# Performance work log

Measured on AMD Instinct MI355X. Metric: run time of the kernel, lower is better.

## Reference

```python
import jax, jax.numpy as jnp
import numpy as np

EXPERT_NUM = 64
EXPERT_USE = 8
AUX_LOSS_LAMBDA = 0.01


def setup_inputs() -> dict:
    key = jax.random.key(0)
    k1, k2 = jax.random.split(key)
    h = jax.random.normal(k1, (4, 4096, 2048), dtype=jnp.float32)
    # nn.Linear(embed_dim, expert_num) weight: [expert_num, embed_dim], ~U(-1/sqrt(d), 1/sqrt(d))
    bound = 1.0 / np.sqrt(2048.0)
    W = jax.random.uniform(k2, (EXPERT_NUM, 2048), dtype=jnp.float32,
                           minval=-bound, maxval=bound)
    return {"h": h, "W": W}


def reference(h, W):
    b, s, d = h.shape
    hf = h.reshape(-1, d)                              # [b*s, d]
    logits = jnp.einsum('nd,ed->ne', hf, W)            # [b*s, E]
    scores = jax.nn.softmax(logits, axis=-1)           # [b*s, E]
    expert_scores, expert_ids = jax.lax.top_k(scores, EXPERT_USE)  # [b*s, k]
    expert_weight = expert_scores / jnp.sum(expert_scores, axis=-1, keepdims=True)
    # L2 load-balance aux loss (training mode, lambda > 0)
    seq_probs = scores.reshape(b, s, EXPERT_NUM).mean(axis=1)      # [b, E]
    aux_loss = jnp.mean(jnp.sum(seq_probs ** 2, axis=-1)) * EXPERT_NUM * AUX_LOSS_LAMBDA
    return expert_ids, expert_weight, aux_loss
```

## Files before the change

kernel.cpp:

```cpp
#include <hip/hip_runtime.h>
#include <math.h>

#define NTOK 16384
#define DIM 2048
#define NEXP 64
#define TOPK 8
#define BT 64
#define KC 64
#define NCHUNK (DIM / KC)
#define PADK 68
#define EPW 4

typedef float f2 __attribute__((ext_vector_type(2)));
typedef float f4 __attribute__((ext_vector_type(4)));

__device__ __forceinline__ f2 pk_mul_sv(f2 bs, f2 av) {
    f2 d; asm("v_pk_mul_f32 %0, %1, %2" : "=v"(d) : "s"(bs), "v"(av)); return d;
}
__device__ __forceinline__ f2 pk_add(f2 a, f2 b) {
    f2 d; asm("v_pk_add_f32 %0, %1, %2" : "=v"(d) : "v"(a), "v"(b)); return d;
}

__global__ __launch_bounds__(512, 4) void moe_gemm(
    const float* __restrict__ h, const float* __restrict__ W,
    float* __restrict__ lgout)
{
#pragma clang fp contract(off)
    __shared__ float sA[2][BT * PADK];

    const int tid  = threadIdx.x;
    const int lane = tid & 63;
    const int wv   = tid >> 6;
    const int tile = blockIdx.x >> 1;
    const int hf   = blockIdx.x & 1;
    const long tok0 = (long)tile * BT;
    const float* hA = h + tok0 * DIM;

    const int e0 = __builtin_amdgcn_readfirstlane(hf * 32 + wv * EPW);
    const float* wb = W + (long)e0 * DIM;

    const int rs0 = tid >> 4;
    const int cs0 = (tid & 15) * 4;

    f4 ra = *(const f4*)(hA + (long)rs0 * DIM + cs0);
    f4 rb = *(const f4*)(hA + (long)(rs0 + 32) * DIM + cs0);
    *(f4*)&sA[0][rs0 * PADK + cs0]        = ra;
    *(f4*)&sA[0][(rs0 + 32) * PADK + cs0] = rb;
    ra = *(const f4*)(hA + (long)rs0 * DIM + KC + cs0);
    rb = *(const f4*)(hA + (long)(rs0 + 32) * DIM + KC + cs0);

    f2 a01[EPW], a23[EPW];
    #pragma unroll
    for (int j = 0; j < EPW; ++j) { a01[j] = (f2)(0.f); a23[j] = (f2)(0.f); }

    for (int kc = 0; kc < NCHUNK; ++kc) {
        __syncthreads();
        const int cur = kc & 1;

        if (kc + 1 < NCHUNK) {
            *(f4*)&sA[cur ^ 1][rs0 * PADK + cs0]        = ra;
            *(f4*)&sA[cur ^ 1][(rs0 + 32) * PADK + cs0] = rb;
        }
        if (kc + 2 < NCHUNK) {
            const long ko = (long)(kc + 2) * KC;
            ra = *(const f4*)(hA + (long)rs0 * DIM + ko + cs0);
            rb = *(const f4*)(hA + (long)(rs0 + 32) * DIM + ko + cs0);
        }

        #pragma unroll
        for (int s = 0; s < 4; ++s) {
            const int kb = kc * KC + s * 16;

            f4 B[EPW][4];
            #pragma unroll
            for (int j = 0; j < EPW; ++j)
                #pragma unroll
                for (int q = 0; q < 4; ++q)
                    B[j][q] = *(const f4*)(wb + (long)j * DIM + kb + 4 * q);

            f4 af[4];
            const float* ab = &sA[cur][lane * PADK + s * 16];
            #pragma unroll
            for (int v = 0; v < 4; ++v) af[v] = *(const f4*)(ab + 4 * v);

            f2 alo[4], ahi[4];
            #pragma unroll
            for (int v = 0; v < 4; ++v) {
                alo[v] = __builtin_shufflevector(af[v], af[v], 0, 1);
                ahi[v] = __builtin_shufflevector(af[v], af[v], 2, 3);
            }

            #pragma unroll
            for (int j = 0; j < EPW; ++j) {
                f2 blo[4], bhi[4];
                #pragma unroll
                for (int v = 0; v < 4; ++v) {
                    blo[v] = __builtin_shufflevector(B[j][v], B[j][v], 0, 1);
                    bhi[v] = __builtin_shufflevector(B[j][v], B[j][v], 2, 3);
                }
                f2 t;
                t = pk_add(pk_mul_sv(blo[3], alo[3]), a01[j]);
                t = pk_add(pk_mul_sv(blo[2], alo[2]), t);
                t = pk_add(pk_mul_sv(blo[1], alo[1]), t);
                a01[j] = pk_add(pk_mul_sv(blo[0], alo[0]), t);
                t = pk_add(pk_mul_sv(bhi[3], ahi[3]), a23[j]);
                t = pk_add(pk_mul_sv(bhi[2], ahi[2]), t);
                t = pk_add(pk_mul_sv(bhi[1], ahi[1]), t);
                a23[j] = pk_add(pk_mul_sv(bhi[0], ahi[0]), t);
            }
        }
    }

    #pragma unroll
    for (int j = 0; j < EPW; ++j) {
        f2 s2 = pk_add(a01[j], a23[j]);
        lgout[(tok0 + lane) * NEXP + e0 + j] = s2.x + s2.y;
    }
}

__global__ __launch_bounds__(512) void softmax_topk(
    const float* __restrict__ lgout, float* __restrict__ out,
    float* __restrict__ wsum)
{
    __shared__ float ls[8][NEXP + 2];
    const int tid  = threadIdx.x;
    const int lane = tid & 63;
    const int wv8  = tid >> 6;
    const int blk  = blockIdx.x;
    const long tok0 = (long)blk * 64;
    float auxacc = 0.f;

    for (int tt = 0; tt < 8; ++tt) {
        const long gt = tok0 + wv8 * 8 + tt;
        const float s = lgout[gt * NEXP + lane];

        float m = s;
        #pragma unroll
        for (int off = 32; off >= 1; off >>= 1)
            m = fmaxf(m, __shfl_xor(m, off));

        const float p = expf(s - m);
        ls[wv8][lane] = p;
        __asm__ volatile("" ::: "memory");

        float r0s = ls[wv8][0], r1s = ls[wv8][1], r2s = ls[wv8][2], r3s = ls[wv8][3];
        float r4s = ls[wv8][4], r5s = ls[wv8][5], r6s = ls[wv8][6], r7s = ls[wv8][7];
        #pragma unroll
        for (int i = 1; i < 8; ++i) {
            r0s += ls[wv8][8 * i + 0]; r1s += ls[wv8][8 * i + 1];
            r2s += ls[wv8][8 * i + 2]; r3s += ls[wv8][8 * i + 3];
            r4s += ls[wv8][8 * i + 4]; r5s += ls[wv8][8 * i + 5];
            r6s += ls[wv8][8 * i + 6]; r7s += ls[wv8][8 * i + 7];
        }
        const float S = ((r0s + r1s) + (r2s + r3s)) + ((r4s + r5s) + (r6s + r7s));

        const float score = p / S;
        auxacc += score;

        float cv = score;
        float myv = 0.f;
        int   myi = 0;
        #pragma unroll
        for (int i = 0; i < TOPK; ++i) {
            float v = cv;
            int idx = lane;
            #pragma unroll
            for (int off = 32; off >= 1; off >>= 1) {
                float v2 = __shfl_xor(v, off);
                int   i2 = __shfl_xor(idx, off);
                if (v2 > v || (v2 == v && i2 < idx)) { v = v2; idx = i2; }
            }
            if (lane == i)   { myv = v; myi = idx; }
            if (lane == idx) cv = -1.f;
        }

        float S8 = 0.f;
        #pragma unroll
        for (int r = 0; r < TOPK; ++r) S8 += __shfl(myv, r);

        if (lane < TOPK) {
            const long o = gt * TOPK + lane;
            out[o]                     = (float)myi;
            out[(long)NTOK * TOPK + o] = myv / S8;
        }
    }

    atomicAdd(&wsum[(blk >> 6) * NEXP + lane], auxacc);
}

__global__ __launch_bounds__(1024, 1) void moe_gate_np(
    const float* __restrict__ h, const float* __restrict__ W,
    float* __restrict__ out, float* __restrict__ wsum)
{
#pragma clang fp contract(off)
    __shared__ float sA[BT * PADK];
    __shared__ float lg[BT][NEXP + 2];

    const int tid  = threadIdx.x;
    const int lane = tid & 63;
    const int wv   = tid >> 6;
    const int blk  = blockIdx.x;
    const long tok0 = (long)blk * BT;
    const float* hA = h + tok0 * DIM;

    const int e0 = __builtin_amdgcn_readfirstlane(wv) * EPW;
    const float* wb = W + (long)e0 * DIM;

    const int rs = tid >> 4;
    const int cs = (tid & 15) * 4;
    f4 pa = *(const f4*)(hA + (long)rs * DIM + cs);

    f2 a01[EPW], a23[EPW];
    #pragma unroll
    for (int j = 0; j < EPW; ++j) { a01[j] = (f2)(0.f); a23[j] = (f2)(0.f); }

    for (int kc = 0; kc < NCHUNK; ++kc) {
        __syncthreads();
        *(f4*)&sA[rs * PADK + cs] = pa;
        __syncthreads();
        if (kc + 1 < NCHUNK)
            pa = *(const f4*)(hA + (long)rs * DIM + (long)(kc + 1) * KC + cs);

        #pragma unroll
        for (int s = 0; s < 4; ++s) {
            const int kb = kc * KC + s * 16;
            f4 B[EPW][4];
            #pragma unroll
            for (int j = 0; j < EPW; ++j)
                #pragma unroll
                for (int q = 0; q < 4; ++q)
                    B[j][q] = *(const f4*)(wb + (long)j * DIM + kb + 4 * q);
            f4 af[4];
            const float* ab = &sA[lane * PADK + s * 16];
            #pragma unroll
            for (int v = 0; v < 4; ++v) af[v] = *(const f4*)(ab + 4 * v);
            f2 alo[4], ahi[4];
            #pragma unroll
            for (int v = 0; v < 4; ++v) {
                alo[v] = __builtin_shufflevector(af[v], af[v], 0, 1);
                ahi[v] = __builtin_shufflevector(af[v], af[v], 2, 3);
            }
            #pragma unroll
            for (int j = 0; j < EPW; ++j) {
                f2 blo[4], bhi[4];
                #pragma unroll
                for (int v = 0; v < 4; ++v) {
                    blo[v] = __builtin_shufflevector(B[j][v], B[j][v], 0, 1);
                    bhi[v] = __builtin_shufflevector(B[j][v], B[j][v], 2, 3);
                }
                f2 t;
                t = pk_add(pk_mul_sv(blo[3], alo[3]), a01[j]);
                t = pk_add(pk_mul_sv(blo[2], alo[2]), t);
                t = pk_add(pk_mul_sv(blo[1], alo[1]), t);
                a01[j] = pk_add(pk_mul_sv(blo[0], alo[0]), t);
                t = pk_add(pk_mul_sv(bhi[3], ahi[3]), a23[j]);
                t = pk_add(pk_mul_sv(bhi[2], ahi[2]), t);
                t = pk_add(pk_mul_sv(bhi[1], ahi[1]), t);
                a23[j] = pk_add(pk_mul_sv(bhi[0], ahi[0]), t);
            }
        }
    }

    #pragma unroll
    for (int j = 0; j < EPW; ++j) {
        f2 s2 = pk_add(a01[j], a23[j]);
        lg[lane][e0 + j] = s2.x + s2.y;
    }
    __syncthreads();

    float auxacc = 0.f;
    for (int tt = 0; tt < 4; ++tt) {
        const int t = wv * 4 + tt;
        const float s = lg[t][lane];
        float m = s;
        #pragma unroll
        for (int off = 32; off >= 1; off >>= 1)
            m = fmaxf(m, __shfl_xor(m, off));
        const float p = expf(s - m);
        lg[t][lane] = p;
        __asm__ volatile("" ::: "memory");
        float r0s = lg[t][0], r1s = lg[t][1], r2s = lg[t][2], r3s = lg[t][3];
        float r4s = lg[t][4], r5s = lg[t][5], r6s = lg[t][6], r7s = lg[t][7];
        #pragma unroll
        for (int i = 1; i < 8; ++i) {
            r0s += lg[t][8 * i + 0]; r1s += lg[t][8 * i + 1];
            r2s += lg[t][8 * i + 2]; r3s += lg[t][8 * i + 3];
            r4s += lg[t][8 * i + 4]; r5s += lg[t][8 * i + 5];
            r6s += lg[t][8 * i + 6]; r7s += lg[t][8 * i + 7];
        }
        const float S = ((r0s + r1s) + (r2s + r3s)) + ((r4s + r5s) + (r6s + r7s));
        const float score = p / S;
        auxacc += score;
        float cv = score;
        float myv = 0.f;
        int   myi = 0;
        #pragma unroll
        for (int i = 0; i < TOPK; ++i) {
            float v = cv;
            int idx = lane;
            #pragma unroll
            for (int off = 32; off >= 1; off >>= 1) {
                float v2 = __shfl_xor(v, off);
                int   i2 = __shfl_xor(idx, off);
                if (v2 > v || (v2 == v && i2 < idx)) { v = v2; idx = i2; }
            }
            if (lane == i)   { myv = v; myi = idx; }
            if (lane == idx) cv = -1.f;
        }
        float S8 = 0.f;
        #pragma unroll
        for (int r = 0; r < TOPK; ++r) S8 += __shfl(myv, r);
        if (lane < TOPK) {
            const long o = (tok0 + t) * TOPK + lane;
            out[o]                     = (float)myi;
            out[(long)NTOK * TOPK + o] = myv / S8;
        }
    }
    atomicAdd(&wsum[(blk >> 6) * NEXP + lane], auxacc);
}

__global__ void aux_finish(const float* __restrict__ wsum, float* __restrict__ out)
{
    const int lane = threadIdx.x;
    float a = 0.f;
    #pragma unroll
    for (int b = 0; b < 4; ++b) {
        const float v = wsum[b * NEXP + lane] * (1.0f / 4096.0f);
        a = fmaf(v, v, a);
    }
    #pragma unroll
    for (int off = 32; off >= 1; off >>= 1)
        a += __shfl_xor(a, off);
    if (lane == 0)
        out[2L * NTOK * TOPK] = a * 0.25f * (float)NEXP * 0.01f;
}

extern "C" void kernel_launch(void* const* d_in, const int* in_sizes, int n_in,
                              void* d_out, int out_size, void* d_ws, size_t ws_size,
                              hipStream_t stream) {
    const float* h = (const float*)d_in[0];
    const float* W = (const float*)d_in[1];
    float* out  = (float*)d_out;
    float* wsum = (float*)d_ws;

    const size_t need = 4096 + (size_t)NTOK * NEXP * sizeof(float);

    hipMemsetAsync(d_ws, 0, 1024, stream);
    if (ws_size >= need) {
        float* lgout = (float*)((char*)d_ws + 4096);
        moe_gemm<<<(NTOK / BT) * 2, 512, 0, stream>>>(h, W, lgout);
        softmax_topk<<<NTOK / 64, 512, 0, stream>>>(lgout, out, wsum);
    } else {
        moe_gate_np<<<NTOK / BT, 1024, 0, stream>>>(h, W, out, wsum);
    }
    aux_finish<<<1, 64, 0, stream>>>(wsum, out);
}
```

Measured before the change: 164.0 us.

## Fuse softmax/top-k and aux-loss finish into GEMM kernel via per-tile completion flags

After: 336.6 us. +105.2%, slower.

```diff
diff --git a/kernel.cpp b/kernel.cpp
--- a/kernel.cpp
+++ b/kernel.cpp
@@ -10,6 +10,7 @@
 #define NCHUNK (DIM / KC)
 #define PADK 68
 #define EPW 4
+#define NTILE (NTOK / BT)
 
 typedef float f2 __attribute__((ext_vector_type(2)));
 typedef float f4 __attribute__((ext_vector_type(4)));
@@ -21,12 +22,15 @@
     f2 d; asm("v_pk_add_f32 %0, %1, %2" : "=v"(d) : "v"(a), "v"(b)); return d;
 }
 
-__global__ __launch_bounds__(512, 4) void moe_gemm(
+__global__ __launch_bounds__(512, 4) void moe_gemm_fused(
     const float* __restrict__ h, const float* __restrict__ W,
-    float* __restrict__ lgout)
+    float* __restrict__ out, float* __restrict__ wsum,
+    int* __restrict__ flags, float* __restrict__ lgout)
 {
 #pragma clang fp contract(off)
     __shared__ float sA[2][BT * PADK];
+    __shared__ float ls[8][NEXP + 2];
+    __shared__ int swin, sdone;
 
     const int tid  = threadIdx.x;
     const int lane = tid & 63;
@@ -116,23 +120,18 @@
         f2 s2 = pk_add(a01[j], a23[j]);
         lgout[(tok0 + lane) * NEXP + e0 + j] = s2.x + s2.y;
     }
-}
-
-__global__ __launch_bounds__(512) void softmax_topk(
-    const float* __restrict__ lgout, float* __restrict__ out,
-    float* __restrict__ wsum)
-{
-    __shared__ float ls[8][NEXP + 2];
-    const int tid  = threadIdx.x;
-    const int lane = tid & 63;
-    const int wv8  = tid >> 6;
-    const int blk  = blockIdx.x;
-    const long tok0 = (long)blk * 64;
+
+    __threadfence();
+    __syncthreads();
+    if (tid == 0) swin = atomicAdd(&flags[tile], 1);
+    __syncthreads();
+    if (swin != 1) return;
+
     float auxacc = 0.f;
-
     for (int tt = 0; tt < 8; ++tt) {
-        const long gt = tok0 + wv8 * 8 + tt;
-        const float s = lgout[gt * NEXP + lane];
+        const long gt = tok0 + wv * 8 + tt;
+        const float s = __hip_atomic_load(&lgout[gt * NEXP + lane],
+                                          __ATOMIC_RELAXED, __HIP_MEMORY_SCOPE_AGENT);
 
         float m = s;
         #pragma unroll
@@ -140,17 +139,17 @@
             m = fmaxf(m, __shfl_xor(m, off));
 
         const float p = expf(s - m);
-        ls[wv8][lane] = p;
+        ls[wv][lane] = p;
         __asm__ volatile("" ::: "memory");
 
-        float r0s = ls[wv8][0], r1s = ls[wv8][1], r2s = ls[wv8][2], r3s = ls[wv8][3];
-        float r4s = ls[wv8][4], r5s = ls[wv8][5], r6s = ls[wv8][6], r7s = ls[wv8][7];
+        float r0s = ls[wv][0], r1s = ls[wv][1], r2s = ls[wv][2], r3s = ls[wv][3];
+        float r4s = ls[wv][4], r5s = ls[wv][5], r6s = ls[wv][6], r7s = ls[wv][7];
         #pragma unroll
         for (int i = 1; i < 8; ++i) {
-            r0s += ls[wv8][8 * i + 0]; r1s += ls[wv8][8 * i + 1];
-            r2s += ls[wv8][8 * i + 2]; r3s += ls[wv8][8 * i + 3];
-            r4s += ls[wv8][8 * i + 4]; r5s += ls[wv8][8 * i + 5];
-            r6s += ls[wv8][8 * i + 6]; r7s += ls[wv8][8 * i + 7];
+            r0s += ls[wv][8 * i + 0]; r1s += ls[wv][8 * i + 1];
+            r2s += ls[wv][8 * i + 2]; r3s += ls[wv][8 * i + 3];
+            r4s += ls[wv][8 * i + 4]; r5s += ls[wv][8 * i + 5];
+            r6s += ls[wv][8 * i + 6]; r7s += ls[wv][8 * i + 7];
         }
         const float S = ((r0s + r1s) + (r2s + r3s)) + ((r4s + r5s) + (r6s + r7s));
 
@@ -184,8 +183,25 @@
             out[(long)NTOK * TOPK + o] = myv / S8;
         }
     }
-
-    atomicAdd(&wsum[(blk >> 6) * NEXP + lane], auxacc);
+    atomicAdd(&wsum[(tile >> 6) * NEXP + lane], auxacc);
+
+    __threadfence();
+    __syncthreads();
+    if (tid == 0) sdone = atomicAdd(&flags[NTILE], 1);
+    __syncthreads();
+    if (sdone == NTILE - 1 && tid < 64) {
+        float a = 0.f;
+        #pragma unroll
+        for (int b = 0; b < 4; ++b) {
+            const float v = atomicAdd(&wsum[b * NEXP + tid], 0.f) * (1.0f / 4096.0f);
+            a = fmaf(v, v, a);
+        }
+        #pragma unroll
+        for (int off = 32; off >= 1; off >>= 1)
+            a += __shfl_xor(a, off);
+        if (tid == 0)
+            out[2L * NTOK * TOPK] = a * 0.25f * (float)NEXP * 0.01f;
+    }
 }
 
 __global__ __launch_bounds__(1024, 1) void moe_gate_np(
@@ -342,16 +358,16 @@
     const float* W = (const float*)d_in[1];
     float* out  = (float*)d_out;
     float* wsum = (float*)d_ws;
-
-    const size_t need = 4096 + (size_t)NTOK * NEXP * sizeof(float);
-
-    hipMemsetAsync(d_ws, 0, 1024, stream);
+    int*   flags = (int*)((char*)d_ws + 4096);
+    float* lgout = (float*)((char*)d_ws + 8192);
+
+    const size_t need = 8192 + (size_t)NTOK * NEXP * sizeof(float);
+
+    hipMemsetAsync(d_ws, 0, 8192, stream);
     if (ws_size >= need) {
-        float* lgout = (float*)((char*)d_ws + 4096);
-        moe_gemm<<<(NTOK / BT) * 2, 512, 0, stream>>>(h, W, lgout);
-        softmax_topk<<<NTOK / 64, 512, 0, stream>>>(lgout, out, wsum);
+        moe_gemm_fused<<<NTILE * 2, 512, 0, stream>>>(h, W, out, wsum, flags, lgout);
     } else {
         moe_gate_np<<<NTOK / BT, 1024, 0, stream>>>(h, W, out, wsum);
-    }
-    aux_finish<<<1, 64, 0, stream>>>(wsum, out);
-}
+        aux_finish<<<1, 64, 0, stream>>>(wsum, out);
+    }
+}
```

## Retile gate GEMM to 128-token tiles with 16 experts per block

Applied to the files above, without the earlier changes.

After: 205.4 us. 25.2% more time.

```diff
diff --git a/kernel.cpp b/kernel.cpp
--- a/kernel.cpp
+++ b/kernel.cpp
@@ -5,11 +5,12 @@
 #define DIM 2048
 #define NEXP 64
 #define TOPK 8
-#define BT 64
-#define KC 64
+#define TT 128
+#define KC 32
 #define NCHUNK (DIM / KC)
-#define PADK 68
+#define PADK 36
 #define EPW 4
+#define NTILE (NTOK / TT)
 
 typedef float f2 __attribute__((ext_vector_type(2)));
 typedef float f4 __attribute__((ext_vector_type(4)));
@@ -21,54 +22,69 @@
     f2 d; asm("v_pk_add_f32 %0, %1, %2" : "=v"(d) : "v"(a), "v"(b)); return d;
 }
 
-__global__ __launch_bounds__(512, 4) void moe_gemm(
+__global__ __launch_bounds__(256, 2) void moe_gemm(
     const float* __restrict__ h, const float* __restrict__ W,
     float* __restrict__ lgout)
 {
 #pragma clang fp contract(off)
-    __shared__ float sA[2][BT * PADK];
+    __shared__ float sA[2][TT * PADK];
 
     const int tid  = threadIdx.x;
     const int lane = tid & 63;
     const int wv   = tid >> 6;
-    const int tile = blockIdx.x >> 1;
-    const int hf   = blockIdx.x & 1;
-    const long tok0 = (long)tile * BT;
+    const int tile = blockIdx.x >> 2;
+    const int qt   = blockIdx.x & 3;
+    const long tok0 = (long)tile * TT;
     const float* hA = h + tok0 * DIM;
 
-    const int e0 = __builtin_amdgcn_readfirstlane(hf * 32 + wv * EPW);
+    const int e0 = __builtin_amdgcn_readfirstlane(qt * 16 + wv * EPW);
     const float* wb = W + (long)e0 * DIM;
 
-    const int rs0 = tid >> 4;
-    const int cs0 = (tid & 15) * 4;
-
-    f4 ra = *(const f4*)(hA + (long)rs0 * DIM + cs0);
-    f4 rb = *(const f4*)(hA + (long)(rs0 + 32) * DIM + cs0);
-    *(f4*)&sA[0][rs0 * PADK + cs0]        = ra;
-    *(f4*)&sA[0][(rs0 + 32) * PADK + cs0] = rb;
-    ra = *(const f4*)(hA + (long)rs0 * DIM + KC + cs0);
-    rb = *(const f4*)(hA + (long)(rs0 + 32) * DIM + KC + cs0);
-
-    f2 a01[EPW], a23[EPW];
-    #pragma unroll
-    for (int j = 0; j < EPW; ++j) { a01[j] = (f2)(0.f); a23[j] = (f2)(0.f); }
+    f4 pa[4];
+    #pragma unroll
+    for (int q = 0; q < 4; ++q) {
+        const int idx = tid + 256 * q;
+        pa[q] = *(const f4*)(hA + (long)(idx >> 3) * DIM + (idx & 7) * 4);
+    }
+    #pragma unroll
+    for (int q = 0; q < 4; ++q) {
+        const int idx = tid + 256 * q;
+        *(f4*)&sA[0][(idx >> 3) * PADK + (idx & 7) * 4] = pa[q];
+    }
+    #pragma unroll
+    for (int q = 0; q < 4; ++q) {
+        const int idx = tid + 256 * q;
+        pa[q] = *(const f4*)(hA + (long)(idx >> 3) * DIM + KC + (idx & 7) * 4);
+    }
+
+    f2 a01[2][EPW], a23[2][EPW];
+    #pragma unroll
+    for (int t = 0; t < 2; ++t)
+        #pragma unroll
+        for (int j = 0; j < EPW; ++j) { a01[t][j] = (f2)(0.f); a23[t][j] = (f2)(0.f); }
 
     for (int kc = 0; kc < NCHUNK; ++kc) {
         __syncthreads();
         const int cur = kc & 1;
 
         if (kc + 1 < NCHUNK) {
-            *(f4*)&sA[cur ^ 1][rs0 * PADK + cs0]        = ra;
-            *(f4*)&sA[cur ^ 1][(rs0 + 32) * PADK + cs0] = rb;
+            #pragma unroll
+            for (int q = 0; q < 4; ++q) {
+                const int idx = tid + 256 * q;
+                *(f4*)&sA[cur ^ 1][(idx >> 3) * PADK + (idx & 7) * 4] = pa[q];
+            }
         }
         if (kc + 2 < NCHUNK) {
             const long ko = (long)(kc + 2) * KC;
-            ra = *(const f4*)(hA + (long)rs0 * DIM + ko + cs0);
-            rb = *(const f4*)(hA + (long)(rs0 + 32) * DIM + ko + cs0);
-        }
-
-        #pragma unroll
-        for (int s = 0; s < 4; ++s) {
+            #pragma unroll
+            for (int q = 0; q < 4; ++q) {
+                const int idx = tid + 256 * q;
+                pa[q] = *(const f4*)(hA + (long)(idx >> 3) * DIM + ko + (idx & 7) * 4);
+            }
+        }
+
+        #pragma unroll
+        for (int s = 0; s < 2; ++s) {
             const int kb = kc * KC + s * 16;
 
             f4 B[EPW][4];
@@ -78,43 +94,53 @@
                 for (int q = 0; q < 4; ++q)
                     B[j][q] = *(const f4*)(wb + (long)j * DIM + kb + 4 * q);
 
-            f4 af[4];
-            const float* ab = &sA[cur][lane * PADK + s * 16];
-            #pragma unroll
-            for (int v = 0; v < 4; ++v) af[v] = *(const f4*)(ab + 4 * v);
-
-            f2 alo[4], ahi[4];
-            #pragma unroll
-            for (int v = 0; v < 4; ++v) {
-                alo[v] = __builtin_shufflevector(af[v], af[v], 0, 1);
-                ahi[v] = __builtin_shufflevector(af[v], af[v], 2, 3);
-            }
-
-            #pragma unroll
-            for (int j = 0; j < EPW; ++j) {
-                f2 blo[4], bhi[4];
+            f4 af[2][4];
+            #pragma unroll
+            for (int t = 0; t < 2; ++t) {
+                const float* ab = &sA[cur][(lane + 64 * t) * PADK + s * 16];
+                #pragma unroll
+                for (int v = 0; v < 4; ++v) af[t][v] = *(const f4*)(ab + 4 * v);
+            }
+
+            #pragma unroll
+            for (int t = 0; t < 2; ++t) {
+                f2 alo[4], ahi[4];
                 #pragma unroll
                 for (int v = 0; v < 4; ++v) {
-                    blo[v] = __builtin_shufflevector(B[j][v], B[j][v], 0, 1);
-                    bhi[v] = __builtin_shufflevector(B[j][v], B[j][v], 2, 3);
+                    alo[v] = __builtin_shufflevector(af[t][v], af[t][v], 0, 1);
+                    ahi[v] = __builtin_shufflevector(af[t][v], af[t][v], 2, 3);
                 }
-                f2 t;
-                t = pk_add(pk_mul_sv(blo[3], alo[3]), a01[j]);
-                t = pk_add(pk_mul_sv(blo[2], alo[2]), t);
-                t = pk_add(pk_mul_sv(blo[1], alo[1]), t);
-                a01[j] = pk_add(pk_mul_sv(blo[0], alo[0]), t);
-                t = pk_add(pk_mul_sv(bhi[3], ahi[3]), a23[j]);
-                t = pk_add(pk_mul_sv(bhi[2], ahi[2]), t);
-                t = pk_add(pk_mul_sv(bhi[1], ahi[1]), t);
-                a23[j] = pk_add(pk_mul_sv(bhi[0], ahi[0]), t);
-            }
-        }
-    }
-
-    #pragma unroll
-    for (int j = 0; j < EPW; ++j) {
-        f2 s2 = pk_add(a01[j], a23[j]);
-        lgout[(tok0 + lane) * NEXP + e0 + j] = s2.x + s2.y;
+                #pragma unroll
+                for (int j = 0; j < EPW; ++j) {
+                    f2 blo[4], bhi[4];
+                    #pragma unroll
+                    for (int v = 0; v < 4; ++v) {
+                        blo[v] = __builtin_shufflevector(B[j][v], B[j][v], 0, 1);
+                        bhi[v] = __builtin_shufflevector(B[j][v], B[j][v], 2, 3);
+                    }
+                    f2 x;
+                    x = pk_add(pk_mul_sv(blo[3], alo[3]), a01[t][j]);
+                    x = pk_add(pk_mul_sv(blo[2], alo[2]), x);
+                    x = pk_add(pk_mul_sv(blo[1], alo[1]), x);
+                    a01[t][j] = pk_add(pk_mul_sv(blo[0], alo[0]), x);
+                    x = pk_add(pk_mul_sv(bhi[3], ahi[3]), a23[t][j]);
+                    x = pk_add(pk_mul_sv(bhi[2], ahi[2]), x);
+                    x = pk_add(pk_mul_sv(bhi[1], ahi[1]), x);
+                    a23[t][j] = pk_add(pk_mul_sv(bhi[0], ahi[0]), x);
+                }
+            }
+        }
+    }
+
+    #pragma unroll
+    for (int t = 0; t < 2; ++t) {
+        f4 o4;
+        #pragma unroll
+        for (int j = 0; j < EPW; ++j) {
+            f2 s2 = pk_add(a01[t][j], a23[t][j]);
+            o4[j] = s2.x + s2.y;
+        }
+        *(f4*)&lgout[(tok0 + lane + 64 * t) * NEXP + e0] = o4;
     }
 }
 
@@ -188,12 +214,31 @@
     atomicAdd(&wsum[(blk >> 6) * NEXP + lane], auxacc);
 }
 
+__global__ void aux_finish(const float* __restrict__ wsum, float* __restrict__ out)
+{
+    const int lane = threadIdx.x;
+    float a = 0.f;
+    #pragma unroll
+    for (int b = 0; b < 4; ++b) {
+        const float v = wsum[b * NEXP + lane] * (1.0f / 4096.0f);
+        a = fmaf(v, v, a);
+    }
+    #pragma unroll
+    for (int off = 32; off >= 1; off >>= 1)
+        a += __shfl_xor(a, off);
+    if (lane == 0)
+        out[2L * NTOK * TOPK] = a * 0.25f * (float)NEXP * 0.01f;
+}
+
+#define BT 64
+#define KCM 64
+#define PADKM 68
 __global__ __launch_bounds__(1024, 1) void moe_gate_np(
     const float* __restrict__ h, const float* __restrict__ W,
     float* __restrict__ out, float* __restrict__ wsum)
 {
 #pragma clang fp contract(off)
-    __shared__ float sA[BT * PADK];
+    __shared__ float sA[BT * PADKM];
     __shared__ float lg[BT][NEXP + 2];
 
     const int tid  = threadIdx.x;
@@ -214,16 +259,16 @@
     #pragma unroll
     for (int j = 0; j < EPW; ++j) { a01[j] = (f2)(0.f); a23[j] = (f2)(0.f); }
 
-    for (int kc = 0; kc < NCHUNK; ++kc) {
+    for (int kc = 0; kc < DIM / KCM; ++kc) {
         __syncthreads();
-        *(f4*)&sA[rs * PADK + cs] = pa;
+        *(f4*)&sA[rs * PADKM + cs] = pa;
         __syncthreads();
-        if (kc + 1 < NCHUNK)
-            pa = *(const f4*)(hA + (long)rs * DIM + (long)(kc + 1) * KC + cs);
+        if (kc + 1 < DIM / KCM)
+            pa = *(const f4*)(hA + (long)rs * DIM + (long)(kc + 1) * KCM + cs);
 
         #pragma unroll
         for (int s = 0; s < 4; ++s) {
-            const int kb = kc * KC + s * 16;
+            const int kb = kc * KCM + s * 16;
             f4 B[EPW][4];
             #pragma unroll
             for (int j = 0; j < EPW; ++j)
@@ -231,7 +276,7 @@
                 for (int q = 0; q < 4; ++q)
                     B[j][q] = *(const f4*)(wb + (long)j * DIM + kb + 4 * q);
             f4 af[4];
-            const float* ab = &sA[lane * PADK + s * 16];
+            const float* ab = &sA[lane * PADKM + s * 16];
             #pragma unroll
             for (int v = 0; v < 4; ++v) af[v] = *(const f4*)(ab + 4 * v);
             f2 alo[4], ahi[4];
@@ -248,15 +293,15 @@
                     blo[v] = __builtin_shufflevector(B[j][v], B[j][v], 0, 1);
                     bhi[v] = __builtin_shufflevector(B[j][v], B[j][v], 2, 3);
                 }
-                f2 t;
-                t = pk_add(pk_mul_sv(blo[3], alo[3]), a01[j]);
-                t = pk_add(pk_mul_sv(blo[2], alo[2]), t);
-                t = pk_add(pk_mul_sv(blo[1], alo[1]), t);
-                a01[j] = pk_add(pk_mul_sv(blo[0], alo[0]), t);
-                t = pk_add(pk_mul_sv(bhi[3], ahi[3]), a23[j]);
-                t = pk_add(pk_mul_sv(bhi[2], ahi[2]), t);
-                t = pk_add(pk_mul_sv(bhi[1], ahi[1]), t);
-                a23[j] = pk_add(pk_mul_sv(bhi[0], ahi[0]), t);
+                f2 x;
+                x = pk_add(pk_mul_sv(blo[3], alo[3]), a01[j]);
+                x = pk_add(pk_mul_sv(blo[2], alo[2]), x);
+                x = pk_add(pk_mul_sv(blo[1], alo[1]), x);
+                a01[j] = pk_add(pk_mul_sv(blo[0], alo[0]), x);
+                x = pk_add(pk_mul_sv(bhi[3], ahi[3]), a23[j]);
+                x = pk_add(pk_mul_sv(bhi[2], ahi[2]), x);
+                x = pk_add(pk_mul_sv(bhi[1], ahi[1]), x);
+                a23[j] = pk_add(pk_mul_sv(bhi[0], ahi[0]), x);
             }
         }
     }
@@ -319,22 +364,6 @@
     atomicAdd(&wsum[(blk >> 6) * NEXP + lane], auxacc);
 }
 
-__global__ void aux_finish(const float* __restrict__ wsum, float* __restrict__ out)
-{
-    const int lane = threadIdx.x;
-    float a = 0.f;
-    #pragma unroll
-    for (int b = 0; b < 4; ++b) {
-        const float v = wsum[b * NEXP + lane] * (1.0f / 4096.0f);
-        a = fmaf(v, v, a);
-    }
-    #pragma unroll
-    for (int off = 32; off >= 1; off >>= 1)
-        a += __shfl_xor(a, off);
-    if (lane == 0)
-        out[2L * NTOK * TOPK] = a * 0.25f * (float)NEXP * 0.01f;
-}
-
 extern "C" void kernel_launch(void* const* d_in, const int* in_sizes, int n_in,
                               void* d_out, int out_size, void* d_ws, size_t ws_size,
                               hipStream_t stream) {
@@ -348,7 +377,7 @@
     hipMemsetAsync(d_ws, 0, 1024, stream);
     if (ws_size >= need) {
         float* lgout = (float*)((char*)d_ws + 4096);
-        moe_gemm<<<(NTOK / BT) * 2, 512, 0, stream>>>(h, W, lgout);
+        moe_gemm<<<NTILE * 4, 256, 0, stream>>>(h, W, lgout);
         softmax_topk<<<NTOK / 64, 512, 0, stream>>>(lgout, out, wsum);
     } else {
         moe_gate_np<<<NTOK / BT, 1024, 0, stream>>>(h, W, out, wsum);
```
